# Kernel optimization log

Hardware: AMD Instinct MI355X
Metric: run time of the kernel (lower is better)

The kernel has to match this reference:

```python
import jax, jax.numpy as jnp
import numpy as np

HEADS = 16
LN_EPS = 1e-5


def setup_inputs() -> dict:
    key = jax.random.key(0)
    k0, k1, k2 = jax.random.split(key, 3)
    B, NE, D = 8, 2048, 1024
    qk_scale = np.sqrt(1.0 / D) * np.sqrt(2.0 / (D + 2 * D))  # xavier_normal gain sqrt(qk_w/D)
    v_scale = np.sqrt(0.01 / D) * np.sqrt(2.0 / (D + D))      # xavier_normal gain sqrt(v_w/D)
    return {
        "inp": jax.random.normal(k0, (B, NE, D), dtype=jnp.float32),
        "gamma": jnp.ones((D,), dtype=jnp.float32),
        "beta": jnp.zeros((D,), dtype=jnp.float32),
        "W_qk": jax.random.normal(k1, (D, 2 * D), dtype=jnp.float32) * qk_scale,
        "b_qk": jnp.zeros((2 * D,), dtype=jnp.float32),
        "W_v": jax.random.normal(k2, (D, D), dtype=jnp.float32) * v_scale,
        "b_v": jnp.zeros((D,), dtype=jnp.float32),
    }


def reference(inp, gamma, beta, W_qk, b_qk, W_v, b_v):
    B, NE, D = inp.shape
    hd = D // HEADS
    # LayerNorm over last dim
    mu = jnp.mean(inp, axis=-1, keepdims=True)
    var = jnp.mean(jnp.square(inp - mu), axis=-1, keepdims=True)
    x = (inp - mu) * jax.lax.rsqrt(var + LN_EPS) * gamma + beta
    # fused qk projection; note interleaved q/k layout in last axis of the view
    qk = (jnp.einsum("bnd,de->bne", x, W_qk) + b_qk).reshape(B, NE, HEADS, hd, 2)
    q = qk[..., 0]  # [B, NE, H, hd]
    k = qk[..., 1]
    v = (jnp.einsum("bnd,de->bne", x, W_v) + b_v).reshape(B, NE, HEADS, hd)
    q = jnp.transpose(q, (0, 2, 1, 3))  # [B, H, NE, hd]
    k = jnp.transpose(k, (0, 2, 3, 1))  # [B, H, hd, NE]
    v = jnp.transpose(v, (0, 2, 1, 3))  # [B, H, NE, hd]
    return (q, k, v)
```

## Files before the change

kernel.cpp:

```cpp
#include <hip/hip_runtime.h>
#include <hip/hip_bf16.h>

#define D_DIM 1024
#define M_TOT 16384
#define N_TOT 3072
#define NQK   2048
#define QKV_SZ 16777216

typedef __attribute__((ext_vector_type(8))) __bf16 bf16x8;
typedef __attribute__((ext_vector_type(4))) float floatx4;

__device__ __forceinline__ unsigned short f2bf(float f) {
  unsigned int u = __float_as_uint(f);
  u += 0x7FFFu + ((u >> 16) & 1u);
  return (unsigned short)(u >> 16);
}

__device__ __forceinline__ void gl2lds16(const void* g, void* l) {
  __builtin_amdgcn_global_load_lds(
      (const __attribute__((address_space(1))) void*)g,
      (__attribute__((address_space(3))) void*)l, 16, 0, 0);
}

__global__ __launch_bounds__(256) void ln_kernel(
    const float* __restrict__ inp, const float* __restrict__ gamma,
    const float* __restrict__ beta, unsigned short* __restrict__ X) {
  const int row = blockIdx.x;
  const int t = threadIdx.x;
  const float* rp = inp + (size_t)row * D_DIM;
  float4 v = *(const float4*)(rp + t * 4);
  float s  = v.x + v.y + v.z + v.w;
  float s2 = v.x * v.x + v.y * v.y + v.z * v.z + v.w * v.w;
#pragma unroll
  for (int o = 1; o < 64; o <<= 1) {
    s  += __shfl_xor(s, o);
    s2 += __shfl_xor(s2, o);
  }
  __shared__ float ws[8];
  const int w = t >> 6, l = t & 63;
  if (l == 0) { ws[w] = s; ws[4 + w] = s2; }
  __syncthreads();
  s  = ws[0] + ws[1] + ws[2] + ws[3];
  s2 = ws[4] + ws[5] + ws[6] + ws[7];
  const float mu = s * (1.0f / D_DIM);
  const float var = s2 * (1.0f / D_DIM) - mu * mu;
  const float rstd = rsqrtf(var + 1e-5f);
  float4 g = *(const float4*)(gamma + t * 4);
  float4 b = *(const float4*)(beta + t * 4);
  ushort4 o;
  o.x = f2bf((v.x - mu) * rstd * g.x + b.x);
  o.y = f2bf((v.y - mu) * rstd * g.y + b.y);
  o.z = f2bf((v.z - mu) * rstd * g.z + b.z);
  o.w = f2bf((v.w - mu) * rstd * g.w + b.w);
  *(ushort4*)(X + (size_t)row * D_DIM + t * 4) = o;
}

__global__ __launch_bounds__(256) void wt_kernel(
    const float* __restrict__ Wqk, const float* __restrict__ Wv,
    unsigned short* __restrict__ Wt) {
  __shared__ float tile[64][65];
  const int n0 = blockIdx.x * 64;
  const int k0 = blockIdx.y * 64;
  const float* src;
  int ldn, nc0;
  if (n0 < NQK) { src = Wqk; ldn = NQK; nc0 = n0; }
  else          { src = Wv;  ldn = D_DIM; nc0 = n0 - NQK; }
  const int t = threadIdx.x;
  const int r = t >> 4;
  const int c4 = (t & 15) << 2;
#pragma unroll
  for (int p = 0; p < 4; ++p) {
    int kk = p * 16 + r;
    float4 vv = *(const float4*)(src + (size_t)(k0 + kk) * ldn + nc0 + c4);
    tile[kk][c4 + 0] = vv.x;
    tile[kk][c4 + 1] = vv.y;
    tile[kk][c4 + 2] = vv.z;
    tile[kk][c4 + 3] = vv.w;
  }
  __syncthreads();
#pragma unroll
  for (int p = 0; p < 4; ++p) {
    int nn = p * 16 + r;
    ushort4 o;
    o.x = f2bf(tile[c4 + 0][nn]);
    o.y = f2bf(tile[c4 + 1][nn]);
    o.z = f2bf(tile[c4 + 2][nn]);
    o.w = f2bf(tile[c4 + 3][nn]);
    *(ushort4*)(Wt + (size_t)(n0 + nn) * D_DIM + k0 + c4) = o;
  }
}

__global__ __launch_bounds__(256) void gemm_kernel(
    const unsigned short* __restrict__ X,
    const unsigned short* __restrict__ Wt,
    const float* __restrict__ bqk, const float* __restrict__ bv,
    float* __restrict__ out) {
  __shared__ __align__(16) unsigned char smem[65536];

  const int bm = blockIdx.x / 24;
  const int bn = blockIdx.x % 24;
  const int m0 = bm * 128;
  const int n0 = bn * 128;
  const int tid = threadIdx.x;
  const int w = tid >> 6, l = tid & 63;
  const int wm = w >> 1, wn = w & 1;
  const int lr = l & 15;
  const int lg = l >> 4;

  const int srow = w * 8 + (l >> 3);
  const int scol = (l & 7) * 8;
  const unsigned short* gA = X  + (size_t)(m0 + srow) * D_DIM + scol;
  const unsigned short* gB = Wt + (size_t)(n0 + srow) * D_DIM + scol;
  const int lbase = w * 1024;

  floatx4 acc[4][4];
#pragma unroll
  for (int i = 0; i < 4; ++i)
#pragma unroll
    for (int j = 0; j < 4; ++j) acc[i][j] = (floatx4){0.f, 0.f, 0.f, 0.f};

#define STAGE(buf, kt)                                                        \
  {                                                                           \
    const int ko_ = (kt) * 64;                                                \
    unsigned char* la_ = smem + (buf) * 16384 + lbase;                        \
    unsigned char* lb_ = smem + 32768 + (buf) * 16384 + lbase;                \
    _Pragma("unroll")                                                         \
    for (int p = 0; p < 4; ++p) {                                             \
      gl2lds16(gA + (size_t)(p * 32) * D_DIM + ko_, la_ + p * 4096);          \
      gl2lds16(gB + (size_t)(p * 32) * D_DIM + ko_, lb_ + p * 4096);          \
    }                                                                         \
  }

#define COMPUTE(buf)                                                          \
  {                                                                           \
    const unsigned short* As_ = (const unsigned short*)(smem + (buf) * 16384);\
    const unsigned short* Bs_ = (const unsigned short*)(smem + 32768 + (buf) * 16384); \
    _Pragma("unroll")                                                         \
    for (int ks = 0; ks < 2; ++ks) {                                          \
      bf16x8 af[4], bf[4];                                                    \
      _Pragma("unroll")                                                       \
      for (int mi = 0; mi < 4; ++mi)                                          \
        af[mi] = *(const bf16x8*)(As_ + (wm * 64 + mi * 16 + lr) * 64 + ks * 32 + lg * 8); \
      _Pragma("unroll")                                                       \
      for (int ni = 0; ni < 4; ++ni)                                          \
        bf[ni] = *(const bf16x8*)(Bs_ + (wn * 64 + ni * 16 + lr) * 64 + ks * 32 + lg * 8); \
      _Pragma("unroll")                                                       \
      for (int mi = 0; mi < 4; ++mi)                                          \
        _Pragma("unroll")                                                     \
        for (int ni = 0; ni < 4; ++ni)                                        \
          acc[mi][ni] = __builtin_amdgcn_mfma_f32_16x16x32_bf16(af[mi], bf[ni], acc[mi][ni], 0, 0, 0); \
    }                                                                         \
  }

  STAGE(0, 0);
  __syncthreads();
  int cur = 0;
#pragma unroll 1
  for (int kt = 0; kt < 15; ++kt) {
    STAGE(cur ^ 1, kt + 1);
    COMPUTE(cur);
    __syncthreads();
    cur ^= 1;
  }
  COMPUTE(cur);

  const size_t OQ = 0, OK = QKV_SZ, OV = 2 * (size_t)QKV_SZ;
  const int bb = m0 >> 11;
  const int mloc = m0 & 2047;
  float* Cf = (float*)smem;

#pragma unroll 1
  for (int pass = 0; pass < 2; ++pass) {
    __syncthreads();
    if (wn == pass) {
#pragma unroll
      for (int ni = 0; ni < 4; ++ni) {
        const int cl = ni * 16 + lr;
        const int ng = n0 + pass * 64 + cl;
        const float bias = (ng < NQK) ? bqk[ng] : bv[ng - NQK];
#pragma unroll
        for (int mi = 0; mi < 4; ++mi) {
          const int r0 = wm * 64 + mi * 16 + lg * 4;
#pragma unroll
          for (int j = 0; j < 4; ++j)
            Cf[(r0 + j) * 65 + cl] = acc[mi][ni][j] + bias;
        }
      }
    }
    __syncthreads();
    if (n0 < NQK) {
      const int h = n0 >> 7;
      {
        const int row = tid >> 1, doff = (tid & 1) * 16;
        const int d0 = pass * 32 + doff;
        float* qp = out + OQ + (((size_t)(bb * 16 + h) * 2048 + mloc + row) * 64) + d0;
        float vbuf[16];
#pragma unroll
        for (int i = 0; i < 16; ++i)
          vbuf[i] = Cf[row * 65 + 2 * (doff + i)];
#pragma unroll
        for (int i4 = 0; i4 < 4; ++i4)
          *(float4*)(qp + i4 * 4) = make_float4(vbuf[i4*4], vbuf[i4*4+1], vbuf[i4*4+2], vbuf[i4*4+3]);
      }
      {
        const int dl = tid >> 3;
        const int neo = (tid & 7) * 16;
        const int d = pass * 32 + dl;
        float* kp = out + OK + (((size_t)(bb * 16 + h) * 64 + d) * 2048) + mloc + neo;
        float vbuf[16];
#pragma unroll
        for (int i = 0; i < 16; ++i)
          vbuf[i] = Cf[(neo + i) * 65 + 2 * dl + 1];
#pragma unroll
        for (int i4 = 0; i4 < 4; ++i4)
          *(float4*)(kp + i4 * 4) = make_float4(vbuf[i4*4], vbuf[i4*4+1], vbuf[i4*4+2], vbuf[i4*4+3]);
      }
    } else {
      const int vbase = (n0 - NQK) + pass * 64;
      const int h = vbase >> 6;
      const int row = tid >> 1, off = (tid & 1) * 32;
      float* vp = out + OV + (((size_t)(bb * 16 + h) * 2048 + mloc + row) * 64) + off;
#pragma unroll
      for (int i4 = 0; i4 < 8; ++i4) {
        float4 t4 = make_float4(Cf[row * 65 + off + i4*4],     Cf[row * 65 + off + i4*4 + 1],
                                Cf[row * 65 + off + i4*4 + 2], Cf[row * 65 + off + i4*4 + 3]);
        *(float4*)(vp + i4 * 4) = t4;
      }
    }
  }
#undef STAGE
#undef COMPUTE
}

extern "C" void kernel_launch(void* const* d_in, const int* in_sizes, int n_in,
                              void* d_out, int out_size, void* d_ws, size_t ws_size,
                              hipStream_t stream) {
  const float* inp   = (const float*)d_in[0];
  const float* gamma = (const float*)d_in[1];
  const float* beta  = (const float*)d_in[2];
  const float* Wqk   = (const float*)d_in[3];
  const float* bqk   = (const float*)d_in[4];
  const float* Wv    = (const float*)d_in[5];
  const float* bv    = (const float*)d_in[6];
  float* out = (float*)d_out;

  unsigned short* X  = (unsigned short*)d_ws;
  unsigned short* Wt = X + (size_t)M_TOT * D_DIM;

  ln_kernel<<<M_TOT, 256, 0, stream>>>(inp, gamma, beta, X);
  wt_kernel<<<dim3(N_TOT / 64, D_DIM / 64), 256, 0, stream>>>(Wqk, Wv, Wt);
  gemm_kernel<<<(M_TOT / 128) * (N_TOT / 128), 256, 0, stream>>>(X, Wt, bqk, bv, out);
}
```

Baseline: 414.2 us.

## Enlarge GEMM tiles to 256x256 with 4-stage swizzled LDS pipeline

The GEMM is restructured to compute 256x256 output tiles with 512 threads (8 waves, each owning 128x64), a K-step of 32, and a four-buffer global-to-LDS ring. The ring is controlled by vmcnt waits and a single barrier per iteration. LDS addresses are XOR-swizzled to reduce bank conflicts, blocks are mapped so each XCD works on neighbouring M rows, and s_setprio is raised around the MFMA bursts. The aim is more data reuse per byte loaded and deeper latency hiding. The cost is 128KB of LDS per block and large accumulator register use, which limits occupancy to one block per CU.

```diff
diff --git a/kernel.cpp b/kernel.cpp
--- a/kernel.cpp
+++ b/kernel.cpp
@@ -90,79 +90,84 @@
   }
 }
 
-__global__ __launch_bounds__(256) void gemm_kernel(
+__global__ __launch_bounds__(512, 2) void gemm_kernel(
     const unsigned short* __restrict__ X,
     const unsigned short* __restrict__ Wt,
     const float* __restrict__ bqk, const float* __restrict__ bv,
     float* __restrict__ out) {
-  __shared__ __align__(16) unsigned char smem[65536];
-
-  const int bm = blockIdx.x / 24;
-  const int bn = blockIdx.x % 24;
-  const int m0 = bm * 128;
-  const int n0 = bn * 128;
+  __shared__ __align__(16) unsigned char smem[131072];
+
+  const int bid = blockIdx.x;
+  const int xcd = bid & 7, tt = bid >> 3;
+  const int bm = xcd * 8 + tt / 12;
+  const int bn = tt % 12;
+  const int m0 = bm * 256, n0 = bn * 256;
+
   const int tid = threadIdx.x;
   const int w = tid >> 6, l = tid & 63;
-  const int wm = w >> 1, wn = w & 1;
-  const int lr = l & 15;
-  const int lg = l >> 4;
-
-  const int srow = w * 8 + (l >> 3);
-  const int scol = (l & 7) * 8;
-  const unsigned short* gA = X  + (size_t)(m0 + srow) * D_DIM + scol;
-  const unsigned short* gB = Wt + (size_t)(n0 + srow) * D_DIM + scol;
-  const int lbase = w * 1024;
-
-  floatx4 acc[4][4];
-#pragma unroll
-  for (int i = 0; i < 4; ++i)
+  const int wm = w >> 2, wn = w & 3;
+  const int lr = l & 15, lg = l >> 4;
+
+  const int rowL = w * 16 + (l >> 2);
+  const int gcol = ((l & 3) ^ ((l >> 3) & 3)) * 8;
+  const unsigned short* gA = X  + (size_t)(m0 + rowL) * D_DIM + gcol;
+  const unsigned short* gB = Wt + (size_t)(n0 + rowL) * D_DIM + gcol;
+  const int ldsW = w * 1024;
+
+  floatx4 acc[8][4];
+#pragma unroll
+  for (int i = 0; i < 8; ++i)
 #pragma unroll
     for (int j = 0; j < 4; ++j) acc[i][j] = (floatx4){0.f, 0.f, 0.f, 0.f};
 
-#define STAGE(buf, kt)                                                        \
+#define STAGE(buf, ktn)                                                       \
   {                                                                           \
-    const int ko_ = (kt) * 64;                                                \
-    unsigned char* la_ = smem + (buf) * 16384 + lbase;                        \
-    unsigned char* lb_ = smem + 32768 + (buf) * 16384 + lbase;                \
-    _Pragma("unroll")                                                         \
-    for (int p = 0; p < 4; ++p) {                                             \
-      gl2lds16(gA + (size_t)(p * 32) * D_DIM + ko_, la_ + p * 4096);          \
-      gl2lds16(gB + (size_t)(p * 32) * D_DIM + ko_, lb_ + p * 4096);          \
-    }                                                                         \
-  }
-
-#define COMPUTE(buf)                                                          \
-  {                                                                           \
-    const unsigned short* As_ = (const unsigned short*)(smem + (buf) * 16384);\
-    const unsigned short* Bs_ = (const unsigned short*)(smem + 32768 + (buf) * 16384); \
-    _Pragma("unroll")                                                         \
-    for (int ks = 0; ks < 2; ++ks) {                                          \
-      bf16x8 af[4], bf[4];                                                    \
-      _Pragma("unroll")                                                       \
-      for (int mi = 0; mi < 4; ++mi)                                          \
-        af[mi] = *(const bf16x8*)(As_ + (wm * 64 + mi * 16 + lr) * 64 + ks * 32 + lg * 8); \
-      _Pragma("unroll")                                                       \
-      for (int ni = 0; ni < 4; ++ni)                                          \
-        bf[ni] = *(const bf16x8*)(Bs_ + (wn * 64 + ni * 16 + lr) * 64 + ks * 32 + lg * 8); \
-      _Pragma("unroll")                                                       \
-      for (int mi = 0; mi < 4; ++mi)                                          \
-        _Pragma("unroll")                                                     \
-        for (int ni = 0; ni < 4; ++ni)                                        \
-          acc[mi][ni] = __builtin_amdgcn_mfma_f32_16x16x32_bf16(af[mi], bf[ni], acc[mi][ni], 0, 0, 0); \
-    }                                                                         \
+    const int kc_ = (ktn) * 32;                                               \
+    unsigned char* base_ = smem + (buf) * 32768;                              \
+    gl2lds16(gA + kc_,                       base_ + ldsW);                   \
+    gl2lds16(gA + (size_t)128 * D_DIM + kc_, base_ + 8192 + ldsW);            \
+    gl2lds16(gB + kc_,                       base_ + 16384 + ldsW);           \
+    gl2lds16(gB + (size_t)128 * D_DIM + kc_, base_ + 24576 + ldsW);           \
   }
 
   STAGE(0, 0);
-  __syncthreads();
-  int cur = 0;
+  STAGE(1, 1);
+  STAGE(2, 2);
+
 #pragma unroll 1
-  for (int kt = 0; kt < 15; ++kt) {
-    STAGE(cur ^ 1, kt + 1);
-    COMPUTE(cur);
-    __syncthreads();
-    cur ^= 1;
-  }
-  COMPUTE(cur);
+  for (int kt = 0; kt < 32; ++kt) {
+    asm volatile("s_waitcnt vmcnt(8)" ::: "memory");
+    __builtin_amdgcn_s_barrier();
+
+    const unsigned char* Ab = smem + (kt & 3) * 32768;
+    const unsigned char* Bb = Ab + 16384;
+
+    bf16x8 bfr[4];
+#pragma unroll
+    for (int ni = 0; ni < 4; ++ni) {
+      int off = (wn * 64 + ni * 16 + lr) * 64 + lg * 16;
+      off ^= ((off >> 7) & 3) << 4;
+      bfr[ni] = *(const bf16x8*)(Bb + off);
+    }
+    bf16x8 afr[8];
+#pragma unroll
+    for (int mi = 0; mi < 8; ++mi) {
+      int off = (wm * 128 + mi * 16 + lr) * 64 + lg * 16;
+      off ^= ((off >> 7) & 3) << 4;
+      afr[mi] = *(const bf16x8*)(Ab + off);
+    }
+
+    STAGE((kt + 3) & 3, (kt + 3) & 31);
+
+    __builtin_amdgcn_s_setprio(1);
+#pragma unroll
+    for (int mi = 0; mi < 8; ++mi)
+#pragma unroll
+      for (int ni = 0; ni < 4; ++ni)
+        acc[mi][ni] = __builtin_amdgcn_mfma_f32_16x16x32_bf16(afr[mi], bfr[ni], acc[mi][ni], 0, 0, 0);
+    __builtin_amdgcn_s_setprio(0);
+  }
+  asm volatile("s_waitcnt vmcnt(0)" ::: "memory");
 
   const size_t OQ = 0, OK = QKV_SZ, OV = 2 * (size_t)QKV_SZ;
   const int bb = m0 >> 11;
@@ -170,7 +175,7 @@
   float* Cf = (float*)smem;
 
 #pragma unroll 1
-  for (int pass = 0; pass < 2; ++pass) {
+  for (int pass = 0; pass < 4; ++pass) {
     __syncthreads();
     if (wn == pass) {
 #pragma unroll
@@ -179,57 +184,54 @@
         const int ng = n0 + pass * 64 + cl;
         const float bias = (ng < NQK) ? bqk[ng] : bv[ng - NQK];
 #pragma unroll
-        for (int mi = 0; mi < 4; ++mi) {
-          const int r0 = wm * 64 + mi * 16 + lg * 4;
+        for (int mi = 0; mi < 8; ++mi) {
+          const int r0 = wm * 128 + mi * 16 + lg * 4;
 #pragma unroll
           for (int j = 0; j < 4; ++j)
-            Cf[(r0 + j) * 65 + cl] = acc[mi][ni][j] + bias;
+            Cf[(r0 + j) * 66 + cl] = acc[mi][ni][j] + bias;
         }
       }
     }
     __syncthreads();
-    if (n0 < NQK) {
-      const int h = n0 >> 7;
+    const int ng0 = n0 + pass * 64;
+    if (ng0 < NQK) {
+      const int h = ng0 >> 7;
+      const int d0p = (ng0 & 127) >> 1;
       {
         const int row = tid >> 1, doff = (tid & 1) * 16;
-        const int d0 = pass * 32 + doff;
-        float* qp = out + OQ + (((size_t)(bb * 16 + h) * 2048 + mloc + row) * 64) + d0;
-        float vbuf[16];
-#pragma unroll
-        for (int i = 0; i < 16; ++i)
-          vbuf[i] = Cf[row * 65 + 2 * (doff + i)];
+        float* qp = out + OQ + (((size_t)(bb * 16 + h) * 2048 + mloc + row) * 64) + d0p + doff;
+        float vb[16];
+#pragma unroll
+        for (int i = 0; i < 16; ++i) vb[i] = Cf[row * 66 + 2 * (doff + i)];
 #pragma unroll
         for (int i4 = 0; i4 < 4; ++i4)
-          *(float4*)(qp + i4 * 4) = make_float4(vbuf[i4*4], vbuf[i4*4+1], vbuf[i4*4+2], vbuf[i4*4+3]);
+          *(float4*)(qp + i4 * 4) = make_float4(vb[i4*4], vb[i4*4+1], vb[i4*4+2], vb[i4*4+3]);
       }
       {
-        const int dl = tid >> 3;
-        const int neo = (tid & 7) * 16;
-        const int d = pass * 32 + dl;
-        float* kp = out + OK + (((size_t)(bb * 16 + h) * 64 + d) * 2048) + mloc + neo;
-        float vbuf[16];
-#pragma unroll
-        for (int i = 0; i < 16; ++i)
-          vbuf[i] = Cf[(neo + i) * 65 + 2 * dl + 1];
+        const int dl = tid >> 4;
+        const int neo = (tid & 15) * 16;
+        float* kp = out + OK + (((size_t)(bb * 16 + h) * 64 + d0p + dl) * 2048) + mloc + neo;
+        float vb[16];
+#pragma unroll
+        for (int i = 0; i < 16; ++i) vb[i] = Cf[(neo + i) * 66 + 2 * dl + 1];
 #pragma unroll
         for (int i4 = 0; i4 < 4; ++i4)
-          *(float4*)(kp + i4 * 4) = make_float4(vbuf[i4*4], vbuf[i4*4+1], vbuf[i4*4+2], vbuf[i4*4+3]);
+          *(float4*)(kp + i4 * 4) = make_float4(vb[i4*4], vb[i4*4+1], vb[i4*4+2], vb[i4*4+3]);
       }
     } else {
-      const int vbase = (n0 - NQK) + pass * 64;
+      const int vbase = ng0 - NQK;
       const int h = vbase >> 6;
       const int row = tid >> 1, off = (tid & 1) * 32;
       float* vp = out + OV + (((size_t)(bb * 16 + h) * 2048 + mloc + row) * 64) + off;
 #pragma unroll
       for (int i4 = 0; i4 < 8; ++i4) {
-        float4 t4 = make_float4(Cf[row * 65 + off + i4*4],     Cf[row * 65 + off + i4*4 + 1],
-                                Cf[row * 65 + off + i4*4 + 2], Cf[row * 65 + off + i4*4 + 3]);
+        float4 t4 = make_float4(Cf[row * 66 + off + i4*4],     Cf[row * 66 + off + i4*4 + 1],
+                                Cf[row * 66 + off + i4*4 + 2], Cf[row * 66 + off + i4*4 + 3]);
         *(float4*)(vp + i4 * 4) = t4;
       }
     }
   }
 #undef STAGE
-#undef COMPUTE
 }
 
 extern "C" void kernel_launch(void* const* d_in, const int* in_sizes, int n_in,
@@ -249,5 +251,5 @@
 
   ln_kernel<<<M_TOT, 256, 0, stream>>>(inp, gamma, beta, X);
   wt_kernel<<<dim3(N_TOT / 64, D_DIM / 64), 256, 0, stream>>>(Wqk, Wv, Wt);
-  gemm_kernel<<<(M_TOT / 128) * (N_TOT / 128), 256, 0, stream>>>(X, Wt, bqk, bv, out);
-}
+  gemm_kernel<<<(M_TOT / 256) * (N_TOT / 256), 512, 0, stream>>>(X, Wt, bqk, bv, out);
+}
```

Result: faster. 400.6 us (-3.3%).
